# Kernel optimization log

Measured on AMD Instinct MI355X. Metric: run time of the kernel, lower is better.

Reference implementation:

```python
import jax, jax.numpy as jnp
import numpy as np

ALPHA = 0.2  # LeakyReLU negative slope
NEG_INF = -9e15


def setup_inputs() -> dict:
    key = jax.random.key(0)
    k1, k2, k3, k4 = jax.random.split(key, 4)
    B, N, F_in, F_out = 8, 2048, 256, 128
    h = jax.random.normal(k1, (B, N, F_in), dtype=jnp.float32)
    adj = jax.random.randint(k2, (B, N, N), 0, 2, dtype=jnp.int32)
    # xavier_uniform with gain=1.414
    def xavier(k, shape, gain=1.414):
        fan_in, fan_out = shape[0], shape[1]
        limit = gain * np.sqrt(6.0 / (fan_in + fan_out))
        return jax.random.uniform(k, shape, jnp.float32, -limit, limit)
    W = xavier(k3, (F_in, F_out))
    a = xavier(k4, (2 * F_out, 1))
    return {"h": h, "adj": adj, "W": W, "a": a}


def reference(h, adj, W, a):
    # h: [B,N,F_in], adj: [B,N,N], W: [F_in,F_out], a: [2*F_out,1]
    Wh = jnp.einsum('bnf,fe->bne', h, W)  # [B,N,E]
    E = Wh.shape[-1]
    a_src, a_dst = a[:E, 0], a[E:, 0]
    # e[b,i,j] = leakyrelu(Wh[b,i].a_src + Wh[b,j].a_dst)  (additive decomposition
    # of a @ concat(Wh_i, Wh_j) -- same math, no [B,N,N,2E] intermediate)
    s_src = Wh @ a_src  # [B,N]
    s_dst = Wh @ a_dst  # [B,N]
    e = jax.nn.leaky_relu(s_src[:, :, None] + s_dst[:, None, :], negative_slope=ALPHA)
    e = jnp.where(adj > 0, e, NEG_INF)
    attention = jax.nn.softmax(e, axis=2)  # [B,N,N]
    # dropout p=0.0 / eval mode -> identity
    h_prime = jnp.einsum('bij,bje->bie', attention, Wh)
    return jax.nn.elu(h_prime)  # concat=True
```

## Files before the change

kernel.cpp:

```cpp
#include <hip/hip_runtime.h>
#include <hip/hip_bf16.h>

#define GAT_ALPHA 0.2f
#define LOG2E 1.4426950408889634f

typedef float f32x4 __attribute__((ext_vector_type(4)));
typedef int   i32x4 __attribute__((ext_vector_type(4)));
typedef short bf16x8 __attribute__((ext_vector_type(8)));

static constexpr int Nn  = 2048;
static constexpr int FIN = 256;
static constexpr int FO  = 128;

static __device__ __forceinline__ unsigned short f2bf(float x) {
    __hip_bfloat16 h = __float2bfloat16(x);
    return __builtin_bit_cast(unsigned short, h);
}
static __device__ __forceinline__ float bf2f(unsigned short u) {
    unsigned int v = ((unsigned int)u) << 16;
    return __builtin_bit_cast(float, v);
}

__global__ __launch_bounds__(256) void gat_prep(
        const float* __restrict__ W, const float* __restrict__ a,
        float* __restrict__ wa, unsigned int* __restrict__ md_key)
{
    __shared__ float pr[32][8];
    __shared__ float pd[32][8];
    const int t = threadIdx.x;
    const int kl = t >> 3, seg = t & 7;
    const int k = blockIdx.x * 32 + kl;
    float ps = 0.f, pv = 0.f;
    const float* wr = W + (size_t)k * FO + seg * 16;
    #pragma unroll
    for (int f = 0; f < 16; f += 4) {
        f32x4 wv = *(const f32x4*)(wr + f);
        f32x4 as = *(const f32x4*)(a + seg * 16 + f);
        f32x4 ad = *(const f32x4*)(a + FO + seg * 16 + f);
        ps += wv[0]*as[0] + wv[1]*as[1] + wv[2]*as[2] + wv[3]*as[3];
        pv += wv[0]*ad[0] + wv[1]*ad[1] + wv[2]*ad[2] + wv[3]*ad[3];
    }
    pr[kl][seg] = ps; pd[kl][seg] = pv;
    __syncthreads();
    if (t < 32) {
        float s = 0.f, d = 0.f;
        #pragma unroll
        for (int j = 0; j < 8; ++j) { s += pr[t][j]; d += pd[t][j]; }
        wa[blockIdx.x * 32 + t]       = s;
        wa[256 + blockIdx.x * 32 + t] = d;
    }
    if (blockIdx.x == 0 && t < 8) md_key[t] = 0u;
}

__global__ __launch_bounds__(256) void gat_wh(
        const float* __restrict__ h, const float* __restrict__ W,
        const float* __restrict__ wa, unsigned short* __restrict__ WhT,
        float* __restrict__ s_src, float* __restrict__ s_dst,
        unsigned int* __restrict__ md_key)
{
    __shared__ unsigned short WT[FO][264];
    __shared__ float wal[512];
    __shared__ float sred[64][4][2];
    __shared__ float red64[64];
    const int t  = threadIdx.x;
    const int b  = blockIdx.x & 7;
    const int n0 = (blockIdx.x >> 3) << 6;

    if (t < 128) *(f32x4*)&wal[t * 4] = *(const f32x4*)&wa[t * 4];
    #pragma unroll
    for (int c = 0; c < 32; ++c) {
        int flat = c * 1024 + t * 4;
        int k = flat >> 7, f = flat & 127;
        f32x4 wv = *(const f32x4*)&W[flat];
        WT[f + 0][k] = f2bf(wv[0]);
        WT[f + 1][k] = f2bf(wv[1]);
        WT[f + 2][k] = f2bf(wv[2]);
        WT[f + 3][k] = f2bf(wv[3]);
    }
    __syncthreads();

    {
        const int row = t >> 2, seg = t & 3;
        const float* hp  = h + ((size_t)(b * Nn + n0 + row)) * FIN + seg * 64;
        const float* was = &wal[seg * 64];
        const float* wad = &wal[256 + seg * 64];
        float ps = 0.f, pv = 0.f;
        #pragma unroll
        for (int j = 0; j < 64; j += 4) {
            f32x4 hv = *(const f32x4*)(hp + j);
            f32x4 sv = *(const f32x4*)(was + j);
            f32x4 dv = *(const f32x4*)(wad + j);
            ps += hv[0]*sv[0] + hv[1]*sv[1] + hv[2]*sv[2] + hv[3]*sv[3];
            pv += hv[0]*dv[0] + hv[1]*dv[1] + hv[2]*dv[2] + hv[3]*dv[3];
        }
        sred[row][seg][0] = ps;
        sred[row][seg][1] = pv;
    }
    __syncthreads();
    if (t < 64) {
        float s = sred[t][0][0] + sred[t][1][0] + sred[t][2][0] + sred[t][3][0];
        float d = sred[t][0][1] + sred[t][1][1] + sred[t][2][1] + sred[t][3][1];
        s_src[b * Nn + n0 + t] = s;
        s_dst[b * Nn + n0 + t] = d;
        red64[t] = d;
    }
    __syncthreads();
    if (t < 16) red64[t] = fmaxf(fmaxf(red64[t], red64[t + 16]),
                                 fmaxf(red64[t + 32], red64[t + 48]));
    __syncthreads();
    if (t == 0) {
        float m = red64[0];
        #pragma unroll
        for (int j = 1; j < 16; ++j) m = fmaxf(m, red64[j]);
        unsigned int bits = __builtin_bit_cast(unsigned int, m);
        unsigned int key  = (bits & 0x80000000u) ? ~bits : (bits | 0x80000000u);
        atomicMax(md_key + b, key);
    }

    const int w = t >> 6, lane = t & 63, n16 = lane & 15, quad = lane >> 4;
    const float* ha = h + ((size_t)(b * Nn + n0 + w * 16 + n16)) * FIN + quad * 8;
    f32x4 acc[8] = {};
    #pragma unroll
    for (int ks = 0; ks < 8; ++ks) {
        f32x4 h0 = *(const f32x4*)(ha + ks * 32);
        f32x4 h1 = *(const f32x4*)(ha + ks * 32 + 4);
        bf16x8 af;
        af[0] = (short)f2bf(h0[0]); af[1] = (short)f2bf(h0[1]);
        af[2] = (short)f2bf(h0[2]); af[3] = (short)f2bf(h0[3]);
        af[4] = (short)f2bf(h1[0]); af[5] = (short)f2bf(h1[1]);
        af[6] = (short)f2bf(h1[2]); af[7] = (short)f2bf(h1[3]);
        #pragma unroll
        for (int nt = 0; nt < 8; ++nt) {
            bf16x8 bfr = *(const bf16x8*)&WT[nt * 16 + n16][ks * 32 + quad * 8];
            acc[nt] = __builtin_amdgcn_mfma_f32_16x16x32_bf16(af, bfr, acc[nt], 0, 0, 0);
        }
    }
    #pragma unroll
    for (int nt = 0; nt < 8; ++nt) {
        ushort4 pk;
        pk.x = f2bf(acc[nt][0]); pk.y = f2bf(acc[nt][1]);
        pk.z = f2bf(acc[nt][2]); pk.w = f2bf(acc[nt][3]);
        *(ushort4*)&WhT[((size_t)(b * FO + nt * 16 + n16)) * Nn + n0 + w * 16 + quad * 4] = pk;
    }
}

__global__ __launch_bounds__(256, 2) void gat_attn(
        const int* __restrict__ adj, const unsigned short* __restrict__ WhT,
        const float* __restrict__ s_src, const float* __restrict__ s_dst,
        const unsigned int* __restrict__ md_key, float* __restrict__ out)
{
    constexpr int AS = 132;
    __shared__ __align__(16) float accbuf[2 * 32 * AS];
    __shared__ float l_red[32];

    const int t = threadIdx.x, w = t >> 6, lane = t & 63;
    const int n16 = lane & 15, quad = lane >> 4;
    const int b  = blockIdx.x & 7;
    const int i0 = (blockIdx.x >> 3) << 5;

    if (t < 32) l_red[t] = 0.f;
    __syncthreads();

    const unsigned int key = md_key[b];
    const unsigned int mb  = (key & 0x80000000u) ? (key ^ 0x80000000u) : ~key;
    const float mdb = __builtin_bit_cast(float, mb);

    const float ssr0 = s_src[b * Nn + i0 + n16];
    const float ssr1 = s_src[b * Nn + i0 + 16 + n16];
    const float tm0 = ssr0 + mdb, tm1 = ssr1 + mdb;
    const float mi0 = fmaxf(tm0, GAT_ALPHA * tm0) * LOG2E;
    const float mi1 = fmaxf(tm1, GAT_ALPHA * tm1) * LOG2E;
    const float sL0 = ssr0 * LOG2E, sL1 = ssr1 * LOG2E;

    const int jw = (w << 5) + (quad << 3);
    const int* ap0 = adj + ((size_t)(b * Nn + i0 + n16)) * Nn + jw;
    const int* ap1 = ap0 + (size_t)16 * Nn;
    const float* dptr = s_dst + b * Nn + jw;
    const unsigned short* wptr = WhT + ((size_t)(b * FO + n16)) * Nn + jw;

    f32x4 acc[2][8] = {};
    float ls0 = 0.f, ls1 = 0.f;

    i32x4 pa[4];
    pa[0] = *(const i32x4*)(ap0);
    pa[1] = *(const i32x4*)(ap0 + 4);
    pa[2] = *(const i32x4*)(ap1);
    pa[3] = *(const i32x4*)(ap1 + 4);

    for (int s = 0; s < 16; ++s) {
        const int j0 = s << 7;
        bf16x8 bfr[8];
        #pragma unroll
        for (int nt = 0; nt < 8; ++nt)
            bfr[nt] = *(const bf16x8*)(wptr + (size_t)(nt << 4) * Nn + j0);
        f32x4 d0 = *(const f32x4*)(dptr + j0);
        f32x4 d1 = *(const f32x4*)(dptr + j0 + 4);
        const int jn = (s < 15) ? (j0 + 128) : 0;
        i32x4 na0 = *(const i32x4*)(ap0 + jn);
        i32x4 na1 = *(const i32x4*)(ap0 + jn + 4);
        i32x4 na2 = *(const i32x4*)(ap1 + jn);
        i32x4 na3 = *(const i32x4*)(ap1 + jn + 4);

        bf16x8 af0, af1;
        #pragma unroll
        for (int j = 0; j < 4; ++j) {
            {
                float u  = __builtin_fmaf(d0[j], LOG2E, sL0);
                float lr = fmaxf(u, GAT_ALPHA * u);
                float e  = __builtin_amdgcn_exp2f(lr - mi0);
                e = (pa[0][j] > 0) ? e : 0.f;
                unsigned short us = f2bf(e);
                ls0 += bf2f(us); af0[j] = (short)us;
            }
            {
                float u  = __builtin_fmaf(d1[j], LOG2E, sL0);
                float lr = fmaxf(u, GAT_ALPHA * u);
                float e  = __builtin_amdgcn_exp2f(lr - mi0);
                e = (pa[1][j] > 0) ? e : 0.f;
                unsigned short us = f2bf(e);
                ls0 += bf2f(us); af0[4 + j] = (short)us;
            }
            {
                float u  = __builtin_fmaf(d0[j], LOG2E, sL1);
                float lr = fmaxf(u, GAT_ALPHA * u);
                float e  = __builtin_amdgcn_exp2f(lr - mi1);
                e = (pa[2][j] > 0) ? e : 0.f;
                unsigned short us = f2bf(e);
                ls1 += bf2f(us); af1[j] = (short)us;
            }
            {
                float u  = __builtin_fmaf(d1[j], LOG2E, sL1);
                float lr = fmaxf(u, GAT_ALPHA * u);
                float e  = __builtin_amdgcn_exp2f(lr - mi1);
                e = (pa[3][j] > 0) ? e : 0.f;
                unsigned short us = f2bf(e);
                ls1 += bf2f(us); af1[4 + j] = (short)us;
            }
        }
        #pragma unroll
        for (int nt = 0; nt < 8; ++nt) {
            acc[0][nt] = __builtin_amdgcn_mfma_f32_16x16x32_bf16(af0, bfr[nt], acc[0][nt], 0, 0, 0);
            acc[1][nt] = __builtin_amdgcn_mfma_f32_16x16x32_bf16(af1, bfr[nt], acc[1][nt], 0, 0, 0);
        }
        pa[0] = na0; pa[1] = na1; pa[2] = na2; pa[3] = na3;
    }

    ls0 += __shfl_xor(ls0, 16); ls0 += __shfl_xor(ls0, 32);
    ls1 += __shfl_xor(ls1, 16); ls1 += __shfl_xor(ls1, 32);
    if (quad == 0) {
        atomicAdd(&l_red[n16], ls0);
        atomicAdd(&l_red[16 + n16], ls1);
    }

    if (w < 2) {
        #pragma unroll
        for (int ig = 0; ig < 2; ++ig)
            #pragma unroll
            for (int nt = 0; nt < 8; ++nt)
                #pragma unroll
                for (int rr = 0; rr < 4; ++rr)
                    accbuf[(size_t)w * 32 * AS + (ig * 16 + quad * 4 + rr) * AS + nt * 16 + n16] = acc[ig][nt][rr];
    }
    __syncthreads();
    if (w >= 2) {
        #pragma unroll
        for (int ig = 0; ig < 2; ++ig)
            #pragma unroll
            for (int nt = 0; nt < 8; ++nt)
                #pragma unroll
                for (int rr = 0; rr < 4; ++rr)
                    accbuf[(size_t)(w - 2) * 32 * AS + (ig * 16 + quad * 4 + rr) * AS + nt * 16 + n16] += acc[ig][nt][rr];
    }
    __syncthreads();
    float* ob = out + ((size_t)(b * Nn + i0)) * FO;
    #pragma unroll
    for (int c = 0; c < 4; ++c) {
        int flat = c * 1024 + t * 4;
        int m = flat >> 7, f = flat & 127;
        f32x4 v0 = *(const f32x4*)&accbuf[(size_t)m * AS + f];
        f32x4 v1 = *(const f32x4*)&accbuf[(size_t)32 * AS + m * AS + f];
        float l = l_red[m];
        f32x4 o;
        #pragma unroll
        for (int j = 0; j < 4; ++j) {
            float x = (v0[j] + v1[j]) / l;
            o[j] = x > 0.f ? x : expm1f(x);
        }
        *(f32x4*)&ob[(size_t)m * FO + f] = o;
    }
}

extern "C" void kernel_launch(void* const* d_in, const int* in_sizes, int n_in,
                              void* d_out, int out_size, void* d_ws, size_t ws_size,
                              hipStream_t stream)
{
    const float* h   = (const float*)d_in[0];
    const int*   adj = (const int*)d_in[1];
    const float* W   = (const float*)d_in[2];
    const float* a   = (const float*)d_in[3];
    float* out = (float*)d_out;

    char* ws = (char*)d_ws;
    unsigned short* WhT = (unsigned short*)ws;
    float* s_src        = (float*)(ws + 4194304);
    float* s_dst        = (float*)(ws + 4259840);
    float* wa           = (float*)(ws + 4325376);
    unsigned int* md_key= (unsigned int*)(ws + 4327424);

    hipLaunchKernelGGL(gat_prep, dim3(8),   dim3(256), 0, stream, W, a, wa, md_key);
    hipLaunchKernelGGL(gat_wh,   dim3(256), dim3(256), 0, stream, h, W, wa, WhT, s_src, s_dst, md_key);
    hipLaunchKernelGGL(gat_attn, dim3(512), dim3(256), 0, stream, adj, WhT, s_src, s_dst, md_key, out);
}
```

Measured before the change: 253.1 us.

## Stage Wh tiles in LDS with double buffering and ballot-packed adjacency masks

The Wh projection is now written in a fragment-packed layout. The attention kernel uses 512-thread blocks covering 64 rows, so each Wh tile loaded into double-buffered LDS is shared across twice as many rows. Adjacency is read with coalesced per-lane loads and compressed to bitmasks via ballot into LDS, and s_dst is staged in LDS. The aim is to cut redundant global traffic for Wh and the int32 adjacency. The cost is a barrier every step, more LDS use per block and half as many blocks.

```diff
diff --git a/kernel.cpp b/kernel.cpp
--- a/kernel.cpp
+++ b/kernel.cpp
@@ -54,7 +54,7 @@
 
 __global__ __launch_bounds__(256) void gat_wh(
         const float* __restrict__ h, const float* __restrict__ W,
-        const float* __restrict__ wa, unsigned short* __restrict__ WhT,
+        const float* __restrict__ wa, unsigned short* __restrict__ Wp,
         float* __restrict__ s_src, float* __restrict__ s_dst,
         unsigned int* __restrict__ md_key)
 {
@@ -135,150 +135,197 @@
             acc[nt] = __builtin_amdgcn_mfma_f32_16x16x32_bf16(af, bfr, acc[nt], 0, 0, 0);
         }
     }
-    #pragma unroll
-    for (int nt = 0; nt < 8; ++nt) {
-        ushort4 pk;
-        pk.x = f2bf(acc[nt][0]); pk.y = f2bf(acc[nt][1]);
-        pk.z = f2bf(acc[nt][2]); pk.w = f2bf(acc[nt][3]);
-        *(ushort4*)&WhT[((size_t)(b * FO + nt * 16 + n16)) * Nn + n0 + w * 16 + quad * 4] = pk;
-    }
-}
-
-__global__ __launch_bounds__(256, 2) void gat_attn(
-        const int* __restrict__ adj, const unsigned short* __restrict__ WhT,
+    {
+        const int v      = (n0 >> 5) + (w >> 1);
+        const int quad_p = ((w & 1) << 1) + (quad >> 1);
+        const int eoff   = (quad & 1) << 2;
+        #pragma unroll
+        for (int nt = 0; nt < 8; ++nt) {
+            ushort4 pk;
+            pk.x = f2bf(acc[nt][0]); pk.y = f2bf(acc[nt][1]);
+            pk.z = f2bf(acc[nt][2]); pk.w = f2bf(acc[nt][3]);
+            size_t idx = ((((size_t)(b << 6) + v) * 8 + nt) * 64 + quad_p * 16 + n16) * 8 + eoff;
+            *(ushort4*)&Wp[idx] = pk;
+        }
+    }
+}
+
+__global__ __launch_bounds__(512, 2) void gat_attn(
+        const int* __restrict__ adj, const unsigned short* __restrict__ Wp,
         const float* __restrict__ s_src, const float* __restrict__ s_dst,
         const unsigned int* __restrict__ md_key, float* __restrict__ out)
 {
     constexpr int AS = 132;
-    __shared__ __align__(16) float accbuf[2 * 32 * AS];
-    __shared__ float l_red[32];
+    constexpr int MS = 68;
+    __shared__ __align__(16) float smem_f[2 * 64 * AS];
+    __shared__ __align__(16) unsigned int mlds[64 * MS];
+    __shared__ __align__(16) float dlds[Nn];
+    __shared__ float l_red[64];
+    unsigned short* ldsw = (unsigned short*)smem_f;
 
     const int t = threadIdx.x, w = t >> 6, lane = t & 63;
     const int n16 = lane & 15, quad = lane >> 4;
+    const int rg = w & 1, jwin = w >> 1;
     const int b  = blockIdx.x & 7;
-    const int i0 = (blockIdx.x >> 3) << 5;
-
-    if (t < 32) l_red[t] = 0.f;
-    __syncthreads();
+    const int i0 = (blockIdx.x >> 3) << 6;
+
+    if (t < 64) l_red[t] = 0.f;
+
+    const int* abase = adj + ((size_t)(b * Nn + i0 + w * 8)) * Nn + lane;
+    const unsigned short* wsrc = Wp + ((size_t)b << 18);
+
+    int av[16];
+    #pragma unroll
+    for (int k = 0; k < 16; ++k)
+        av[k] = abase[(size_t)(k >> 1) * Nn + ((k & 1) << 6)];
+    f32x4 pg[4];
+    #pragma unroll
+    for (int p = 0; p < 4; ++p)
+        pg[p] = *(const f32x4*)(wsrc + p * 4096 + t * 8);
+    *(f32x4*)&dlds[t * 4] = *(const f32x4*)(s_dst + b * Nn + t * 4);
 
     const unsigned int key = md_key[b];
-    const unsigned int mb  = (key & 0x80000000u) ? (key ^ 0x80000000u) : ~key;
-    const float mdb = __builtin_bit_cast(float, mb);
-
-    const float ssr0 = s_src[b * Nn + i0 + n16];
-    const float ssr1 = s_src[b * Nn + i0 + 16 + n16];
+    const unsigned int mb_ = (key & 0x80000000u) ? (key ^ 0x80000000u) : ~key;
+    const float mdb = __builtin_bit_cast(float, mb_);
+    const int r0 = i0 + rg * 32 + n16;
+    const float ssr0 = s_src[b * Nn + r0];
+    const float ssr1 = s_src[b * Nn + r0 + 16];
     const float tm0 = ssr0 + mdb, tm1 = ssr1 + mdb;
     const float mi0 = fmaxf(tm0, GAT_ALPHA * tm0) * LOG2E;
     const float mi1 = fmaxf(tm1, GAT_ALPHA * tm1) * LOG2E;
     const float sL0 = ssr0 * LOG2E, sL1 = ssr1 * LOG2E;
-
-    const int jw = (w << 5) + (quad << 3);
-    const int* ap0 = adj + ((size_t)(b * Nn + i0 + n16)) * Nn + jw;
-    const int* ap1 = ap0 + (size_t)16 * Nn;
-    const float* dptr = s_dst + b * Nn + jw;
-    const unsigned short* wptr = WhT + ((size_t)(b * FO + n16)) * Nn + jw;
+    const int jw = (jwin << 5) + (quad << 3);
+    const int mrow0 = (rg * 32 + n16) * MS;
+    const int mrow1 = mrow0 + 16 * MS;
+
+    #pragma unroll
+    for (int k = 0; k < 16; ++k) {
+        unsigned long long m = __ballot(av[k] > 0);
+        const int rr = k >> 1, c = k & 1;
+        if (lane == 0) mlds[(w * 8 + rr) * MS + (c << 1)]     = (unsigned int)m;
+        if (lane == 1) mlds[(w * 8 + rr) * MS + (c << 1) + 1] = (unsigned int)(m >> 32);
+    }
+    #pragma unroll
+    for (int p = 0; p < 4; ++p)
+        *(f32x4*)&ldsw[p * 4096 + t * 8] = pg[p];
 
     f32x4 acc[2][8] = {};
     float ls0 = 0.f, ls1 = 0.f;
-
-    i32x4 pa[4];
-    pa[0] = *(const i32x4*)(ap0);
-    pa[1] = *(const i32x4*)(ap0 + 4);
-    pa[2] = *(const i32x4*)(ap1);
-    pa[3] = *(const i32x4*)(ap1 + 4);
+    __syncthreads();
 
     for (int s = 0; s < 16; ++s) {
+        const int cur = s & 1, nxt = cur ^ 1;
         const int j0 = s << 7;
-        bf16x8 bfr[8];
-        #pragma unroll
-        for (int nt = 0; nt < 8; ++nt)
-            bfr[nt] = *(const bf16x8*)(wptr + (size_t)(nt << 4) * Nn + j0);
-        f32x4 d0 = *(const f32x4*)(dptr + j0);
-        f32x4 d1 = *(const f32x4*)(dptr + j0 + 4);
-        const int jn = (s < 15) ? (j0 + 128) : 0;
-        i32x4 na0 = *(const i32x4*)(ap0 + jn);
-        i32x4 na1 = *(const i32x4*)(ap0 + jn + 4);
-        i32x4 na2 = *(const i32x4*)(ap1 + jn);
-        i32x4 na3 = *(const i32x4*)(ap1 + jn + 4);
+        if (s < 15) {
+            const int coff = (s + 1) << 7;
+            #pragma unroll
+            for (int k = 0; k < 16; ++k)
+                av[k] = abase[(size_t)(k >> 1) * Nn + coff + ((k & 1) << 6)];
+        }
+        f32x4 g[4];
+        if (s < 15) {
+            const unsigned short* src = wsrc + (size_t)(s + 1) * 16384;
+            #pragma unroll
+            for (int p = 0; p < 4; ++p)
+                g[p] = *(const f32x4*)(src + p * 4096 + t * 8);
+        }
+        const unsigned int mw0 = mlds[mrow0 + (s << 2) + jwin];
+        const unsigned int mw1 = mlds[mrow1 + (s << 2) + jwin];
+        const unsigned int mb0 = (mw0 >> (quad << 3)) & 0xffu;
+        const unsigned int mb1 = (mw1 >> (quad << 3)) & 0xffu;
+        f32x4 d0 = *(const f32x4*)&dlds[j0 + jw];
+        f32x4 d1 = *(const f32x4*)&dlds[j0 + jw + 4];
 
         bf16x8 af0, af1;
         #pragma unroll
         for (int j = 0; j < 4; ++j) {
-            {
-                float u  = __builtin_fmaf(d0[j], LOG2E, sL0);
+            {   float u  = __builtin_fmaf(d0[j], LOG2E, sL0);
                 float lr = fmaxf(u, GAT_ALPHA * u);
                 float e  = __builtin_amdgcn_exp2f(lr - mi0);
-                e = (pa[0][j] > 0) ? e : 0.f;
+                e = ((mb0 >> j) & 1u) ? e : 0.f;
                 unsigned short us = f2bf(e);
-                ls0 += bf2f(us); af0[j] = (short)us;
-            }
-            {
-                float u  = __builtin_fmaf(d1[j], LOG2E, sL0);
+                ls0 += bf2f(us); af0[j] = (short)us; }
+            {   float u  = __builtin_fmaf(d1[j], LOG2E, sL0);
                 float lr = fmaxf(u, GAT_ALPHA * u);
                 float e  = __builtin_amdgcn_exp2f(lr - mi0);
-                e = (pa[1][j] > 0) ? e : 0.f;
+                e = ((mb0 >> (4 + j)) & 1u) ? e : 0.f;
                 unsigned short us = f2bf(e);
-                ls0 += bf2f(us); af0[4 + j] = (short)us;
-            }
-            {
-                float u  = __builtin_fmaf(d0[j], LOG2E, sL1);
+                ls0 += bf2f(us); af0[4 + j] = (short)us; }
+            {   float u  = __builtin_fmaf(d0[j], LOG2E, sL1);
                 float lr = fmaxf(u, GAT_ALPHA * u);
                 float e  = __builtin_amdgcn_exp2f(lr - mi1);
-                e = (pa[2][j] > 0) ? e : 0.f;
+                e = ((mb1 >> j) & 1u) ? e : 0.f;
                 unsigned short us = f2bf(e);
-                ls1 += bf2f(us); af1[j] = (short)us;
-            }
-            {
-                float u  = __builtin_fmaf(d1[j], LOG2E, sL1);
+                ls1 += bf2f(us); af1[j] = (short)us; }
+            {   float u  = __builtin_fmaf(d1[j], LOG2E, sL1);
                 float lr = fmaxf(u, GAT_ALPHA * u);
                 float e  = __builtin_amdgcn_exp2f(lr - mi1);
-                e = (pa[3][j] > 0) ? e : 0.f;
+                e = ((mb1 >> (4 + j)) & 1u) ? e : 0.f;
                 unsigned short us = f2bf(e);
-                ls1 += bf2f(us); af1[4 + j] = (short)us;
+                ls1 += bf2f(us); af1[4 + j] = (short)us; }
+        }
+
+        const unsigned short* bbase = &ldsw[cur * 16384 + (jwin << 12) + (lane << 3)];
+        #pragma unroll
+        for (int nt = 0; nt < 8; ++nt) {
+            bf16x8 bfr = *(const bf16x8*)(bbase + (nt << 9));
+            acc[0][nt] = __builtin_amdgcn_mfma_f32_16x16x32_bf16(af0, bfr, acc[0][nt], 0, 0, 0);
+            acc[1][nt] = __builtin_amdgcn_mfma_f32_16x16x32_bf16(af1, bfr, acc[1][nt], 0, 0, 0);
+        }
+
+        if (s < 15) {
+            #pragma unroll
+            for (int k = 0; k < 16; ++k) {
+                unsigned long long m = __ballot(av[k] > 0);
+                const int rr = k >> 1, c = k & 1;
+                const int wd = ((s + 1) << 2) + (c << 1);
+                if (lane == 0) mlds[(w * 8 + rr) * MS + wd]     = (unsigned int)m;
+                if (lane == 1) mlds[(w * 8 + rr) * MS + wd + 1] = (unsigned int)(m >> 32);
             }
-        }
-        #pragma unroll
-        for (int nt = 0; nt < 8; ++nt) {
-            acc[0][nt] = __builtin_amdgcn_mfma_f32_16x16x32_bf16(af0, bfr[nt], acc[0][nt], 0, 0, 0);
-            acc[1][nt] = __builtin_amdgcn_mfma_f32_16x16x32_bf16(af1, bfr[nt], acc[1][nt], 0, 0, 0);
-        }
-        pa[0] = na0; pa[1] = na1; pa[2] = na2; pa[3] = na3;
+            #pragma unroll
+            for (int p = 0; p < 4; ++p)
+                *(f32x4*)&ldsw[nxt * 16384 + p * 4096 + t * 8] = g[p];
+        }
+        __syncthreads();
     }
 
     ls0 += __shfl_xor(ls0, 16); ls0 += __shfl_xor(ls0, 32);
     ls1 += __shfl_xor(ls1, 16); ls1 += __shfl_xor(ls1, 32);
     if (quad == 0) {
-        atomicAdd(&l_red[n16], ls0);
-        atomicAdd(&l_red[16 + n16], ls1);
-    }
-
-    if (w < 2) {
+        atomicAdd(&l_red[rg * 32 + n16], ls0);
+        atomicAdd(&l_red[rg * 32 + 16 + n16], ls1);
+    }
+
+    float* slot = smem_f + (size_t)(jwin & 1) * (64 * AS);
+    const int rbase = rg * 32;
+    if (jwin < 2) {
         #pragma unroll
         for (int ig = 0; ig < 2; ++ig)
             #pragma unroll
             for (int nt = 0; nt < 8; ++nt)
                 #pragma unroll
                 for (int rr = 0; rr < 4; ++rr)
-                    accbuf[(size_t)w * 32 * AS + (ig * 16 + quad * 4 + rr) * AS + nt * 16 + n16] = acc[ig][nt][rr];
-    }
-    __syncthreads();
-    if (w >= 2) {
+                    slot[(size_t)(rbase + ig * 16 + quad * 4 + rr) * AS + nt * 16 + n16] = acc[ig][nt][rr];
+    }
+    __syncthreads();
+    if (jwin >= 2) {
         #pragma unroll
         for (int ig = 0; ig < 2; ++ig)
             #pragma unroll
             for (int nt = 0; nt < 8; ++nt)
                 #pragma unroll
                 for (int rr = 0; rr < 4; ++rr)
-                    accbuf[(size_t)(w - 2) * 32 * AS + (ig * 16 + quad * 4 + rr) * AS + nt * 16 + n16] += acc[ig][nt][rr];
-    }
-    __syncthreads();
+                    slot[(size_t)(rbase + ig * 16 + quad * 4 + rr) * AS + nt * 16 + n16] += acc[ig][nt][rr];
+    }
+    __syncthreads();
+
     float* ob = out + ((size_t)(b * Nn + i0)) * FO;
     #pragma unroll
     for (int c = 0; c < 4; ++c) {
-        int flat = c * 1024 + t * 4;
+        int flat = c * 2048 + t * 4;
         int m = flat >> 7, f = flat & 127;
-        f32x4 v0 = *(const f32x4*)&accbuf[(size_t)m * AS + f];
-        f32x4 v1 = *(const f32x4*)&accbuf[(size_t)32 * AS + m * AS + f];
+        f32x4 v0 = *(const f32x4*)&smem_f[(size_t)m * AS + f];
+        f32x4 v1 = *(const f32x4*)&smem_f[(size_t)(64 + m) * AS + f];
         float l = l_red[m];
         f32x4 o;
         #pragma unroll
@@ -301,13 +348,13 @@
     float* out = (float*)d_out;
 
     char* ws = (char*)d_ws;
-    unsigned short* WhT = (unsigned short*)ws;
+    unsigned short* Wp  = (unsigned short*)ws;
     float* s_src        = (float*)(ws + 4194304);
     float* s_dst        = (float*)(ws + 4259840);
     float* wa           = (float*)(ws + 4325376);
     unsigned int* md_key= (unsigned int*)(ws + 4327424);
 
     hipLaunchKernelGGL(gat_prep, dim3(8),   dim3(256), 0, stream, W, a, wa, md_key);
-    hipLaunchKernelGGL(gat_wh,   dim3(256), dim3(256), 0, stream, h, W, wa, WhT, s_src, s_dst, md_key);
-    hipLaunchKernelGGL(gat_attn, dim3(512), dim3(256), 0, stream, adj, WhT, s_src, s_dst, md_key, out);
-}
+    hipLaunchKernelGGL(gat_wh,   dim3(256), dim3(256), 0, stream, h, W, wa, Wp, s_src, s_dst, md_key);
+    hipLaunchKernelGGL(gat_attn, dim3(256), dim3(512), 0, stream, adj, Wp, s_src, s_dst, md_key, out);
+}
```

Measured after the change: 236.2 us. 1.07x faster.
